# Kernel optimization log

Measured on AMD Instinct MI355X. Metric: run time of the kernel, lower is better.

The kernel has to match this reference:

```python
import jax, jax.numpy as jnp
import numpy as np

ALPHA = 0.2          # LeakyReLU negative slope
NEG_BIG = -9e15      # mask value from original code


def setup_inputs() -> dict:
    key = jax.random.key(0)
    k1, k2, k3, k4 = jax.random.split(key, 4)
    B, N, F_in, F_out = 16, 1024, 256, 256
    x = jax.random.normal(k1, (B, N, F_in), dtype=jnp.float32)
    adj = jax.random.randint(k2, (B, N, N), 0, 2, dtype=jnp.int32)
    # xavier-uniform-like scales
    W = jax.random.normal(k3, (F_in, F_out), dtype=jnp.float32) * np.sqrt(2.0 / (F_in + F_out))
    a = jax.random.normal(k4, (2 * F_out, 1), dtype=jnp.float32) * np.sqrt(2.0 / (2 * F_out + 1))
    return {"x": x, "adj": adj, "W": W, "a": a}


def reference(x, adj, W, a):
    # x: [B,N,Fin], adj: [B,N,N] (int mask), W: [Fin,Fout], a: [2*Fout,1]
    F_out = a.shape[0] // 2
    h = jnp.einsum("bni,io->bno", x, W)            # [B,N,Fout]
    # Decompose a into left/right halves: e_ij = lrelu(a_l.h_i + a_r.h_j)
    a_l = a[:F_out, 0]                               # [Fout]
    a_r = a[F_out:, 0]                               # [Fout]
    el = h @ a_l                                     # [B,N] score contribution of target i
    er = h @ a_r                                     # [B,N] score contribution of source j
    e = jax.nn.leaky_relu(el[:, :, None] + er[:, None, :], ALPHA)  # [B,N,N]
    e = jnp.where(adj > 0, e, NEG_BIG)
    attn = jax.nn.softmax(e, axis=-1)                # masked softmax over neighbors j
    # weighted sum of neighbor features; concat with n_heads=1 is identity
    return jnp.einsum("bij,bjo->bio", attn, h)       # [B,N,Fout]
```

## Files before the change

kernel.cpp:

```cpp
#include <hip/hip_runtime.h>
#include <stdint.h>

#define ALPHA 0.2f
#define NEG_BIG -9000000000000000.0f

typedef __attribute__((ext_vector_type(8))) short bf16x8;
typedef __attribute__((ext_vector_type(8))) unsigned short u16x8;
typedef __attribute__((ext_vector_type(4))) float f32x4;

__device__ __forceinline__ unsigned short f2bf(float f) {
    unsigned int u = __float_as_uint(f);
    u += 0x7fffu + ((u >> 16) & 1u);
    return (unsigned short)(u >> 16);
}

__device__ __forceinline__ void gload_lds16(const void* g, void* l) {
    __builtin_amdgcn_global_load_lds(
        (const __attribute__((address_space(1))) unsigned int*)g,
        (__attribute__((address_space(3))) unsigned int*)l, 16, 0, 0);
}

__global__ void wt_wa_kernel(const float* __restrict__ W,
                             const float* __restrict__ a,
                             unsigned short* __restrict__ Wtbf,
                             float* __restrict__ wa) {
    const int t = threadIdx.x;
    if (blockIdx.x < 256) {
        const int o = blockIdx.x;
        Wtbf[o * 256 + t] = f2bf(W[t * 256 + o]);
    } else {
        float sl = 0.f, sr = 0.f;
        const float* wr = W + t * 256;
        for (int o = 0; o < 256; ++o) {
            const float wv = wr[o];
            sl += wv * a[o];
            sr += wv * a[256 + o];
        }
        wa[t] = sl;
        wa[256 + t] = sr;
    }
}

__global__ __launch_bounds__(256) void eler2x_kernel(
    const float* __restrict__ x, const float* __restrict__ wa,
    float* __restrict__ el, float* __restrict__ er,
    unsigned short* __restrict__ xbf)
{
    const int w = threadIdx.x >> 6, l = threadIdx.x & 63;
    const int r = blockIdx.x * 4 + w;
    const float4 xv = *(const float4*)(x + (size_t)r * 256 + l * 4);
    const float4 al = *(const float4*)(wa + l * 4);
    const float4 ar = *(const float4*)(wa + 256 + l * 4);

    ushort4 xb;
    xb.x = f2bf(xv.x); xb.y = f2bf(xv.y); xb.z = f2bf(xv.z); xb.w = f2bf(xv.w);
    *(ushort4*)(xbf + (size_t)r * 256 + l * 4) = xb;

    float sl = xv.x * al.x + xv.y * al.y + xv.z * al.z + xv.w * al.w;
    float sr = xv.x * ar.x + xv.y * ar.y + xv.z * ar.z + xv.w * ar.w;
#pragma unroll
    for (int off = 32; off >= 1; off >>= 1) {
        sl += __shfl_xor(sl, off);
        sr += __shfl_xor(sr, off);
    }
    if (l == 0) { el[r] = sl; er[r] = sr; }
}

__global__ __launch_bounds__(256) void gemm_bt(
    const unsigned short* __restrict__ A,
    const unsigned short* __restrict__ Bt,
    unsigned short* __restrict__ C,
    int M, int N, int K,
    long long sA, long long sB, long long sC)
{
    __shared__ __align__(16) unsigned short As[128 * 32];
    __shared__ __align__(16) unsigned short Bs[128 * 32];

    const int tid = threadIdx.x;
    const int w = tid >> 6;
    const int l = tid & 63;
    const int q = l >> 4;
    const int ml = l & 15;
    const int wm = (w >> 1) * 64;
    const int wn = (w & 1) * 64;

    const int m0 = blockIdx.y * 128;
    const int n0 = blockIdx.x * 128;
    const unsigned short* Ab = A + (size_t)blockIdx.z * sA;
    const unsigned short* Bb = Bt + (size_t)blockIdx.z * sB;
    unsigned short* Cb = C + (size_t)blockIdx.z * sC;

    f32x4 acc[4][4];
    for (int i = 0; i < 4; ++i)
        for (int j = 0; j < 4; ++j) {
            f32x4 z = {0.f, 0.f, 0.f, 0.f};
            acc[i][j] = z;
        }

    for (int k0 = 0; k0 < K; k0 += 32) {
        for (int c = 0; c < 2; ++c) {
            const int cb = c * 256 + (w << 6);
            const int chunk = cb + l;
            const int r  = chunk >> 2;
            const int co = (chunk & 3) << 3;
            gload_lds16(Ab + (size_t)(m0 + r) * K + k0 + co, As + cb * 8);
            gload_lds16(Bb + (size_t)(n0 + r) * K + k0 + co, Bs + cb * 8);
        }
        __syncthreads();

        bf16x8 aF[4], bF[4];
        for (int mt = 0; mt < 4; ++mt)
            aF[mt] = *(const bf16x8*)(As + (wm + mt * 16 + ml) * 32 + q * 8);
        for (int nt = 0; nt < 4; ++nt)
            bF[nt] = *(const bf16x8*)(Bs + (wn + nt * 16 + ml) * 32 + q * 8);
        for (int mt = 0; mt < 4; ++mt)
            for (int nt = 0; nt < 4; ++nt)
                acc[mt][nt] = __builtin_amdgcn_mfma_f32_16x16x32_bf16(
                    aF[mt], bF[nt], acc[mt][nt], 0, 0, 0);
        __syncthreads();
    }

    for (int mt = 0; mt < 4; ++mt)
        for (int nt = 0; nt < 4; ++nt) {
            const int gn = n0 + wn + nt * 16 + ml;
            for (int r = 0; r < 4; ++r) {
                const int gm = m0 + wm + mt * 16 + q * 4 + r;
                Cb[(size_t)gm * N + gn] = f2bf(acc[mt][nt][r]);
            }
        }
}

__global__ __launch_bounds__(256) void mask_kernel(
    const int* __restrict__ adj,
    const float* __restrict__ el,
    const float* __restrict__ er,
    float* __restrict__ c,
    unsigned short* __restrict__ pk16)
{
    __shared__ unsigned char nibs[4][256];

    const int w = threadIdx.x >> 6, l = threadIdx.x & 63;
    const int row = blockIdx.x * 4 + w;
    const int b = row >> 10;
    const int* arow = adj + (size_t)row * 1024;
    const float* erb = er + (b << 10);
    const float eli = el[row];

    float ev[16];
    float m = -3.0e38f;
#pragma unroll
    for (int it = 0; it < 4; ++it) {
        const int j = it * 256 + l * 4;
        const int4 av = *(const int4*)(arow + j);
        const float4 erv = *(const float4*)(erb + j);
        float e0 = eli + erv.x; e0 = e0 > 0.f ? e0 : ALPHA * e0; e0 = av.x > 0 ? e0 : NEG_BIG;
        float e1 = eli + erv.y; e1 = e1 > 0.f ? e1 : ALPHA * e1; e1 = av.y > 0 ? e1 : NEG_BIG;
        float e2 = eli + erv.z; e2 = e2 > 0.f ? e2 : ALPHA * e2; e2 = av.z > 0 ? e2 : NEG_BIG;
        float e3 = eli + erv.w; e3 = e3 > 0.f ? e3 : ALPHA * e3; e3 = av.w > 0 ? e3 : NEG_BIG;
        ev[it * 4 + 0] = e0; ev[it * 4 + 1] = e1;
        ev[it * 4 + 2] = e2; ev[it * 4 + 3] = e3;
        m = fmaxf(m, fmaxf(fmaxf(e0, e1), fmaxf(e2, e3)));
        nibs[w][it * 64 + l] =
            (unsigned char)((av.x > 0) | ((av.y > 0) << 1) |
                            ((av.z > 0) << 2) | ((av.w > 0) << 3));
    }
#pragma unroll
    for (int off = 32; off >= 1; off >>= 1) m = fmaxf(m, __shfl_xor(m, off));
    float s = 0.f;
#pragma unroll
    for (int u = 0; u < 16; ++u) s += __expf(ev[u] - m);
#pragma unroll
    for (int off = 32; off >= 1; off >>= 1) s += __shfl_xor(s, off);
    if (l == 0) c[row] = m + __logf(s);

    const unsigned nr = *(const unsigned int*)(&nibs[w][l * 4]);
    const unsigned short mask16 =
        (unsigned short)((nr & 0xFu) | ((nr >> 4) & 0xF0u) |
                         ((nr >> 8) & 0xF00u) | ((nr >> 12) & 0xF000u));
    pk16[(size_t)row * 64 + l] = mask16;
}

__global__ __launch_bounds__(256) void pv_kernel(
    const unsigned short* __restrict__ pk16,
    const float* __restrict__ el,
    const float* __restrict__ er,
    const float* __restrict__ c,
    const unsigned short* __restrict__ h_t,
    float* __restrict__ out)
{
    __shared__ float er_s[1024];
    __shared__ __align__(16) unsigned short pk_s[32 * 64];
    __shared__ __align__(16) unsigned short Hs[256 * 32];
    __shared__ __align__(16) unsigned short Ps[32 * 40];

    const int tid = threadIdx.x;
    const int w = tid >> 6, l = tid & 63;
    const int q = l >> 4, ml = l & 15;
    const int b = blockIdx.y;
    const int i0 = blockIdx.x * 32;

    *(float4*)(er_s + tid * 4) = *(const float4*)(er + (b << 10) + tid * 4);
    *(u16x8*)(pk_s + tid * 8) =
        *(const u16x8*)(pk16 + ((size_t)(b << 10) + i0) * 64 + tid * 8);
    const int ib = tid >> 3;
    const int js = (tid & 7) * 4;
    const float eli_b = el[(b << 10) + i0 + ib];
    const float ci = c[(b << 10) + i0 + ib];
    __syncthreads();

    f32x4 acc[2][4];
    for (int i = 0; i < 2; ++i)
        for (int j = 0; j < 4; ++j) {
            f32x4 z = {0.f, 0.f, 0.f, 0.f};
            acc[i][j] = z;
        }

    const unsigned short* hb = h_t + (size_t)b * 262144;

    for (int j0 = 0; j0 < 1024; j0 += 32) {
        for (int cc = 0; cc < 4; ++cc) {
            const int cb = cc * 256 + (w << 6);
            const int chunk = cb + l;
            const int r  = chunk >> 2;
            const int co = (chunk & 3) << 3;
            gload_lds16(hb + (size_t)r * 1024 + j0 + co, Hs + cb * 8);
        }
        {
            const unsigned hw = pk_s[ib * 64 + ((j0 + js) >> 4)];
            const unsigned v = (hw >> ((j0 + js) & 15)) & 0xFu;
            ushort4 pvv;
            float e;
            e = eli_b + er_s[j0 + js + 0]; e = e > 0.f ? e : ALPHA * e;
            pvv.x = (v & 1u) ? f2bf(__expf(e - ci)) : (unsigned short)0;
            e = eli_b + er_s[j0 + js + 1]; e = e > 0.f ? e : ALPHA * e;
            pvv.y = (v & 2u) ? f2bf(__expf(e - ci)) : (unsigned short)0;
            e = eli_b + er_s[j0 + js + 2]; e = e > 0.f ? e : ALPHA * e;
            pvv.z = (v & 4u) ? f2bf(__expf(e - ci)) : (unsigned short)0;
            e = eli_b + er_s[j0 + js + 3]; e = e > 0.f ? e : ALPHA * e;
            pvv.w = (v & 8u) ? f2bf(__expf(e - ci)) : (unsigned short)0;
            *(ushort4*)(Ps + ib * 40 + js) = pvv;
        }
        __syncthreads();

        bf16x8 aF[2], bF[4];
        for (int mt = 0; mt < 2; ++mt)
            aF[mt] = *(const bf16x8*)(Ps + (mt * 16 + ml) * 40 + q * 8);
        for (int nt = 0; nt < 4; ++nt)
            bF[nt] = *(const bf16x8*)(Hs + ((w << 6) + nt * 16 + ml) * 32 + q * 8);
        for (int mt = 0; mt < 2; ++mt)
            for (int nt = 0; nt < 4; ++nt)
                acc[mt][nt] = __builtin_amdgcn_mfma_f32_16x16x32_bf16(
                    aF[mt], bF[nt], acc[mt][nt], 0, 0, 0);
        __syncthreads();
    }

    float* ob = out + (size_t)b * 262144;
    for (int mt = 0; mt < 2; ++mt)
        for (int nt = 0; nt < 4; ++nt) {
            const int gn = (w << 6) + nt * 16 + ml;
            for (int r = 0; r < 4; ++r) {
                const int gm = i0 + mt * 16 + q * 4 + r;
                ob[(size_t)gm * 256 + gn] = acc[mt][nt][r];
            }
        }
}

extern "C" void kernel_launch(void* const* d_in, const int* in_sizes, int n_in,
                              void* d_out, int out_size, void* d_ws, size_t ws_size,
                              hipStream_t stream) {
    const float* x   = (const float*)d_in[0];
    const int*   adj = (const int*)d_in[1];
    const float* W   = (const float*)d_in[2];
    const float* a   = (const float*)d_in[3];
    float* out = (float*)d_out;

    char* ws = (char*)d_ws;
    unsigned short* Wtbf  = (unsigned short*)(ws);
    float* wa             = (float*)(ws + 131072);
    unsigned short* xbf   = (unsigned short*)(ws + 133120);
    unsigned short* h_t   = (unsigned short*)(ws + 8521728);
    float* el             = (float*)(ws + 16910336);
    float* er             = (float*)(ws + 16975872);
    float* c              = (float*)(ws + 17041408);
    unsigned short* pk16  = (unsigned short*)(ws + 17106944);

    wt_wa_kernel<<<dim3(257), dim3(256), 0, stream>>>(W, a, Wtbf, wa);

    eler2x_kernel<<<dim3(4096), dim3(256), 0, stream>>>(x, wa, el, er, xbf);

    gemm_bt<<<dim3(8, 2, 16), dim3(256), 0, stream>>>(
        Wtbf, xbf, h_t, 256, 1024, 256, 0LL, 1024LL * 256, 256LL * 1024);

    mask_kernel<<<dim3(4096), dim3(256), 0, stream>>>(adj, el, er, c, pk16);

    pv_kernel<<<dim3(32, 16), dim3(256), 0, stream>>>(pk16, el, er, c, h_t, out);
}
```

Before: 163.0 us.

## Flatten h GEMM across batches, double K-tile and swizzle LDS in GEMM and PV

The batched h GEMM becomes a single flat GEMM over all 16384 rows, with 64x128 tiles and a K step of 64, and writes h transposed in a [256,16384] layout. The GEMM and the PV kernel both use an XOR-swizzled LDS layout to avoid bank conflicts. PV now processes 64 neighbours per iteration, which halves the number of barrier-separated steps. The cost is larger LDS use per block (Hs grows to 32KB), which may lower occupancy.

```diff
diff --git a/kernel.cpp b/kernel.cpp
--- a/kernel.cpp
+++ b/kernel.cpp
@@ -66,66 +66,75 @@
     if (l == 0) { el[r] = sl; er[r] = sr; }
 }
 
-__global__ __launch_bounds__(256) void gemm_bt(
+__global__ __launch_bounds__(256) void gemm_h(
     const unsigned short* __restrict__ A,
     const unsigned short* __restrict__ Bt,
-    unsigned short* __restrict__ C,
-    int M, int N, int K,
-    long long sA, long long sB, long long sC)
+    unsigned short* __restrict__ C)
 {
-    __shared__ __align__(16) unsigned short As[128 * 32];
-    __shared__ __align__(16) unsigned short Bs[128 * 32];
+    __shared__ __align__(16) unsigned short As[64 * 64];
+    __shared__ __align__(16) unsigned short Bs[128 * 64];
 
     const int tid = threadIdx.x;
-    const int w = tid >> 6;
-    const int l = tid & 63;
-    const int q = l >> 4;
-    const int ml = l & 15;
-    const int wm = (w >> 1) * 64;
+    const int w = tid >> 6, l = tid & 63;
+    const int q = l >> 4, ml = l & 15;
+    const int wm = (w >> 1) * 32;
     const int wn = (w & 1) * 64;
-
-    const int m0 = blockIdx.y * 128;
+    const int m0 = blockIdx.y * 64;
     const int n0 = blockIdx.x * 128;
-    const unsigned short* Ab = A + (size_t)blockIdx.z * sA;
-    const unsigned short* Bb = Bt + (size_t)blockIdx.z * sB;
-    unsigned short* Cb = C + (size_t)blockIdx.z * sC;
-
-    f32x4 acc[4][4];
-    for (int i = 0; i < 4; ++i)
+
+    f32x4 acc[2][4];
+    for (int i = 0; i < 2; ++i)
         for (int j = 0; j < 4; ++j) {
             f32x4 z = {0.f, 0.f, 0.f, 0.f};
             acc[i][j] = z;
         }
 
-    for (int k0 = 0; k0 < K; k0 += 32) {
+    for (int k0 = 0; k0 < 256; k0 += 64) {
         for (int c = 0; c < 2; ++c) {
             const int cb = c * 256 + (w << 6);
-            const int chunk = cb + l;
-            const int r  = chunk >> 2;
-            const int co = (chunk & 3) << 3;
-            gload_lds16(Ab + (size_t)(m0 + r) * K + k0 + co, As + cb * 8);
-            gload_lds16(Bb + (size_t)(n0 + r) * K + k0 + co, Bs + cb * 8);
+            const int p = cb + l;
+            const int r = p >> 3;
+            const int cc = (p & 7) ^ (r & 7);
+            gload_lds16(A + (size_t)(m0 + r) * 256 + k0 + cc * 8, As + cb * 8);
+        }
+        for (int c = 0; c < 4; ++c) {
+            const int cb = c * 256 + (w << 6);
+            const int p = cb + l;
+            const int r = p >> 3;
+            const int cc = (p & 7) ^ (r & 7);
+            gload_lds16(Bt + (size_t)(n0 + r) * 256 + k0 + cc * 8, Bs + cb * 8);
         }
         __syncthreads();
 
-        bf16x8 aF[4], bF[4];
-        for (int mt = 0; mt < 4; ++mt)
-            aF[mt] = *(const bf16x8*)(As + (wm + mt * 16 + ml) * 32 + q * 8);
-        for (int nt = 0; nt < 4; ++nt)
-            bF[nt] = *(const bf16x8*)(Bs + (wn + nt * 16 + ml) * 32 + q * 8);
-        for (int mt = 0; mt < 4; ++mt)
-            for (int nt = 0; nt < 4; ++nt)
-                acc[mt][nt] = __builtin_amdgcn_mfma_f32_16x16x32_bf16(
-                    aF[mt], bF[nt], acc[mt][nt], 0, 0, 0);
+        bf16x8 aF[2][2], bF[2][4];
+#pragma unroll
+        for (int ks = 0; ks < 2; ++ks) {
+#pragma unroll
+            for (int mt = 0; mt < 2; ++mt) {
+                const int mm = wm + mt * 16 + ml;
+                aF[ks][mt] = *(const bf16x8*)(As + (mm * 8 + ((ks * 4 + q) ^ (mm & 7))) * 8);
+            }
+#pragma unroll
+            for (int nt = 0; nt < 4; ++nt) {
+                const int nn = wn + nt * 16 + ml;
+                bF[ks][nt] = *(const bf16x8*)(Bs + (nn * 8 + ((ks * 4 + q) ^ (nn & 7))) * 8);
+            }
+        }
+#pragma unroll
+        for (int ks = 0; ks < 2; ++ks)
+            for (int mt = 0; mt < 2; ++mt)
+                for (int nt = 0; nt < 4; ++nt)
+                    acc[mt][nt] = __builtin_amdgcn_mfma_f32_16x16x32_bf16(
+                        aF[ks][mt], bF[ks][nt], acc[mt][nt], 0, 0, 0);
         __syncthreads();
     }
 
-    for (int mt = 0; mt < 4; ++mt)
+    for (int mt = 0; mt < 2; ++mt)
         for (int nt = 0; nt < 4; ++nt) {
             const int gn = n0 + wn + nt * 16 + ml;
             for (int r = 0; r < 4; ++r) {
                 const int gm = m0 + wm + mt * 16 + q * 4 + r;
-                Cb[(size_t)gm * N + gn] = f2bf(acc[mt][nt][r]);
+                C[(size_t)gm * 16384 + gn] = f2bf(acc[mt][nt][r]);
             }
         }
 }
@@ -185,13 +194,13 @@
     const float* __restrict__ el,
     const float* __restrict__ er,
     const float* __restrict__ c,
-    const unsigned short* __restrict__ h_t,
+    const unsigned short* __restrict__ hT,
     float* __restrict__ out)
 {
     __shared__ float er_s[1024];
     __shared__ __align__(16) unsigned short pk_s[32 * 64];
-    __shared__ __align__(16) unsigned short Hs[256 * 32];
-    __shared__ __align__(16) unsigned short Ps[32 * 40];
+    __shared__ __align__(16) unsigned short Hs[256 * 64];
+    __shared__ __align__(16) unsigned short Ps[32 * 72];
 
     const int tid = threadIdx.x;
     const int w = tid >> 6, l = tid & 63;
@@ -203,7 +212,7 @@
     *(u16x8*)(pk_s + tid * 8) =
         *(const u16x8*)(pk16 + ((size_t)(b << 10) + i0) * 64 + tid * 8);
     const int ib = tid >> 3;
-    const int js = (tid & 7) * 4;
+    const int js = (tid & 7) * 8;
     const float eli_b = el[(b << 10) + i0 + ib];
     const float ci = c[(b << 10) + i0 + ib];
     __syncthreads();
@@ -215,42 +224,49 @@
             acc[i][j] = z;
         }
 
-    const unsigned short* hb = h_t + (size_t)b * 262144;
-
-    for (int j0 = 0; j0 < 1024; j0 += 32) {
-        for (int cc = 0; cc < 4; ++cc) {
-            const int cb = cc * 256 + (w << 6);
-            const int chunk = cb + l;
-            const int r  = chunk >> 2;
-            const int co = (chunk & 3) << 3;
-            gload_lds16(hb + (size_t)r * 1024 + j0 + co, Hs + cb * 8);
+    const unsigned short* hb = hT + (size_t)b * 1024;
+
+    for (int j0 = 0; j0 < 1024; j0 += 64) {
+        for (int cr = 0; cr < 8; ++cr) {
+            const int cb = cr * 256 + (w << 6);
+            const int p = cb + l;
+            const int r = p >> 3;
+            const int cc = (p & 7) ^ (r & 7);
+            gload_lds16(hb + (size_t)r * 16384 + j0 + cc * 8, Hs + cb * 8);
         }
         {
             const unsigned hw = pk_s[ib * 64 + ((j0 + js) >> 4)];
-            const unsigned v = (hw >> ((j0 + js) & 15)) & 0xFu;
-            ushort4 pvv;
-            float e;
-            e = eli_b + er_s[j0 + js + 0]; e = e > 0.f ? e : ALPHA * e;
-            pvv.x = (v & 1u) ? f2bf(__expf(e - ci)) : (unsigned short)0;
-            e = eli_b + er_s[j0 + js + 1]; e = e > 0.f ? e : ALPHA * e;
-            pvv.y = (v & 2u) ? f2bf(__expf(e - ci)) : (unsigned short)0;
-            e = eli_b + er_s[j0 + js + 2]; e = e > 0.f ? e : ALPHA * e;
-            pvv.z = (v & 4u) ? f2bf(__expf(e - ci)) : (unsigned short)0;
-            e = eli_b + er_s[j0 + js + 3]; e = e > 0.f ? e : ALPHA * e;
-            pvv.w = (v & 8u) ? f2bf(__expf(e - ci)) : (unsigned short)0;
-            *(ushort4*)(Ps + ib * 40 + js) = pvv;
+            const unsigned v = (hw >> ((j0 + js) & 15)) & 0xFFu;
+            u16x8 pvv;
+#pragma unroll
+            for (int u = 0; u < 8; ++u) {
+                float e = eli_b + er_s[j0 + js + u];
+                e = e > 0.f ? e : ALPHA * e;
+                const float p = ((v >> u) & 1u) ? __expf(e - ci) : 0.f;
+                pvv[u] = f2bf(p);
+            }
+            *(u16x8*)(Ps + ib * 72 + js) = pvv;
         }
         __syncthreads();
 
-        bf16x8 aF[2], bF[4];
-        for (int mt = 0; mt < 2; ++mt)
-            aF[mt] = *(const bf16x8*)(Ps + (mt * 16 + ml) * 40 + q * 8);
-        for (int nt = 0; nt < 4; ++nt)
-            bF[nt] = *(const bf16x8*)(Hs + ((w << 6) + nt * 16 + ml) * 32 + q * 8);
-        for (int mt = 0; mt < 2; ++mt)
-            for (int nt = 0; nt < 4; ++nt)
-                acc[mt][nt] = __builtin_amdgcn_mfma_f32_16x16x32_bf16(
-                    aF[mt], bF[nt], acc[mt][nt], 0, 0, 0);
+        bf16x8 aF[2][2], bF[2][4];
+#pragma unroll
+        for (int ks = 0; ks < 2; ++ks) {
+#pragma unroll
+            for (int mt = 0; mt < 2; ++mt)
+                aF[ks][mt] = *(const bf16x8*)(Ps + (mt * 16 + ml) * 72 + ks * 32 + q * 8);
+#pragma unroll
+            for (int nt = 0; nt < 4; ++nt) {
+                const int oc = (w << 6) + nt * 16 + ml;
+                bF[ks][nt] = *(const bf16x8*)(Hs + (oc * 8 + ((ks * 4 + q) ^ (oc & 7))) * 8);
+            }
+        }
+#pragma unroll
+        for (int ks = 0; ks < 2; ++ks)
+            for (int mt = 0; mt < 2; ++mt)
+                for (int nt = 0; nt < 4; ++nt)
+                    acc[mt][nt] = __builtin_amdgcn_mfma_f32_16x16x32_bf16(
+                        aF[ks][mt], bF[ks][nt], acc[mt][nt], 0, 0, 0);
         __syncthreads();
     }
 
@@ -278,7 +294,7 @@
     unsigned short* Wtbf  = (unsigned short*)(ws);
     float* wa             = (float*)(ws + 131072);
     unsigned short* xbf   = (unsigned short*)(ws + 133120);
-    unsigned short* h_t   = (unsigned short*)(ws + 8521728);
+    unsigned short* h_T   = (unsigned short*)(ws + 8521728);
     float* el             = (float*)(ws + 16910336);
     float* er             = (float*)(ws + 16975872);
     float* c              = (float*)(ws + 17041408);
@@ -288,10 +304,9 @@
 
     eler2x_kernel<<<dim3(4096), dim3(256), 0, stream>>>(x, wa, el, er, xbf);
 
-    gemm_bt<<<dim3(8, 2, 16), dim3(256), 0, stream>>>(
-        Wtbf, xbf, h_t, 256, 1024, 256, 0LL, 1024LL * 256, 256LL * 1024);
+    gemm_h<<<dim3(128, 4), dim3(256), 0, stream>>>(Wtbf, xbf, h_T);
 
     mask_kernel<<<dim3(4096), dim3(256), 0, stream>>>(adj, el, er, c, pk16);
 
-    pv_kernel<<<dim3(32, 16), dim3(256), 0, stream>>>(pk16, el, er, c, h_t, out);
-}
+    pv_kernel<<<dim3(32, 16), dim3(256), 0, stream>>>(pk16, el, er, c, h_T, out);
+}
```

After: 155.1 us. -4.8%, faster.
